# Performance work log

Hardware: AMD Instinct MI355X
Metric: run time of the kernel (lower is better)

## Reference

```python
import jax, jax.numpy as jnp
import numpy as np

TOP_K = 2
INIT_STD = 0.02
B, T, D, E, I = 2, 2048, 1024, 8, 512


def setup_inputs() -> dict:
    key = jax.random.key(0)
    k0, k1, k2, k3, k4 = jax.random.split(key, 5)
    return {
        "x": jax.random.normal(k0, (B, T, D), dtype=jnp.float32),
        "router_w": (jax.random.normal(k1, (E, D), dtype=jnp.float32) * INIT_STD),
        "w_gate": (jax.random.normal(k2, (E, I, D), dtype=jnp.float32) * INIT_STD),
        "w_up": (jax.random.normal(k3, (E, I, D), dtype=jnp.float32) * INIT_STD),
        "w_down": (jax.random.normal(k4, (E, D, I), dtype=jnp.float32) * INIT_STD),
    }


def _moe_forward(x, router_w, w_gate, w_up, w_down):
    # x: [B, T, D]; router_w: [E, D]; w_gate/w_up: [E, I, D]; w_down: [E, D, I]
    b, t, d = x.shape
    e = router_w.shape[0]
    gate_logits = jnp.einsum('btd,ed->bte', x, router_w)          # [B, T, E]
    top_w, sel = jax.lax.top_k(gate_logits, TOP_K)                # [B, T, K]
    probs = jax.nn.softmax(top_w, axis=-1)                        # softmax over selected experts only

    n = b * t
    xf = x.reshape(n, d)                                          # [N, D]
    sel_f = sel.reshape(n, TOP_K)
    probs_f = probs.reshape(n, TOP_K)
    # combine weights per (token, expert); zero for unselected experts
    gates = jnp.zeros((n, e), dtype=x.dtype).at[
        jnp.arange(n)[:, None], sel_f].add(probs_f)               # [N, E]

    # SwiGLU expert FFN (no bias). Gated-dense formulation: unselected experts
    # have gate weight exactly 0, so this is bit-for-bit the same math as
    # dispatch + grouped GEMM + combine. scan over experts keeps memory at
    # one [N, I] intermediate at a time.
    def body(acc, ws):
        wg, wu, wd, g = ws                                        # [I,D],[I,D],[D,I],[N]
        h = jax.nn.silu(xf @ wg.T) * (xf @ wu.T)                  # [N, I]
        return acc + g[:, None] * (h @ wd.T), None

    out, _ = jax.lax.scan(body, jnp.zeros((n, d), dtype=x.dtype),
                          (w_gate, w_up, w_down, gates.T))
    return out.reshape(b, t, d), gate_logits


def reference(x, router_w, w_gate, w_up, w_down):
    return _moe_forward(x, router_w, w_gate, w_up, w_down)
```

## Files before the change

### kernel.cpp

```cpp
#include <hip/hip_runtime.h>
#include <cstdint>

#define N_TOK 4096
#define D_    1024
#define E_    8
#define I_    512
#define KTOP  2
#define PAD   64
#define BK    64
#define CAP   (N_TOK*KTOP + E_*PAD)
#define NBX   (CAP / PAD)
#define WSZ   ((size_t)E_ * I_ * D_)

typedef __attribute__((ext_vector_type(4))) float f32x4;
typedef __attribute__((ext_vector_type(8))) short bf16x8;

__device__ inline unsigned short f2bf(float f) {
  union { float f; uint32_t u; } v; v.f = f;
  uint32_t r = v.u + 0x7fffu + ((v.u >> 16) & 1u);
  return (unsigned short)(r >> 16);
}
__device__ inline float bf2f(unsigned short h) {
  union { uint32_t u; float f; } v; v.u = ((uint32_t)h) << 16;
  return v.f;
}

#define GLOAD_LDS16(gp, lp)                                                        \
  __builtin_amdgcn_global_load_lds((const __attribute__((address_space(1))) void*)(gp), \
                                   (__attribute__((address_space(3))) void*)(lp), 16, 0, 0)

__global__ __launch_bounds__(256) void convertw_kernel(const float* __restrict__ wg,
                                                       const float* __restrict__ wu,
                                                       const float* __restrict__ wd,
                                                       unsigned short* __restrict__ dst) {
  const int y = blockIdx.y;
  const float* s = (y == 0) ? wg : (y == 1) ? wu : wd;
  unsigned short* d = dst + (size_t)y * WSZ;
  int i = blockIdx.x * 256 + threadIdx.x;
  const float4 v = reinterpret_cast<const float4*>(s)[i];
  ushort4 o;
  o.x = f2bf(v.x); o.y = f2bf(v.y); o.z = f2bf(v.z); o.w = f2bf(v.w);
  reinterpret_cast<ushort4*>(d)[i] = o;
}

__global__ __launch_bounds__(256) void router_kernel(const float* __restrict__ x,
                                                     const float* __restrict__ rw,
                                                     float* __restrict__ logits,
                                                     int* __restrict__ sel,
                                                     float* __restrict__ prob,
                                                     unsigned short* __restrict__ Xb) {
  const int lane = threadIdx.x & 63;
  const int tok  = blockIdx.x * 4 + (threadIdx.x >> 6);
  const float4* xr = reinterpret_cast<const float4*>(x + (size_t)tok * D_);
  float4 xv[4];
#pragma unroll
  for (int q = 0; q < 4; ++q) xv[q] = xr[q * 64 + lane];
  float acc[E_];
#pragma unroll
  for (int e = 0; e < E_; ++e) {
    const float4* wr = reinterpret_cast<const float4*>(rw + (size_t)e * D_);
    float s = 0.f;
#pragma unroll
    for (int q = 0; q < 4; ++q) {
      float4 wv = wr[q * 64 + lane];
      s += xv[q].x * wv.x + xv[q].y * wv.y + xv[q].z * wv.z + xv[q].w * wv.w;
    }
    acc[e] = s;
  }
  ushort4* xb = reinterpret_cast<ushort4*>(Xb + (size_t)tok * D_);
#pragma unroll
  for (int q = 0; q < 4; ++q) {
    ushort4 o;
    o.x = f2bf(xv[q].x); o.y = f2bf(xv[q].y); o.z = f2bf(xv[q].z); o.w = f2bf(xv[q].w);
    xb[q * 64 + lane] = o;
  }
#pragma unroll
  for (int e = 0; e < E_; ++e)
#pragma unroll
    for (int off = 32; off; off >>= 1) acc[e] += __shfl_xor(acc[e], off);
  if (lane == 0) {
    float v0 = -1e30f, v1 = -1e30f; int i0 = 0, i1 = 0;
#pragma unroll
    for (int e = 0; e < E_; ++e) {
      float v = acc[e];
      logits[(size_t)tok * E_ + e] = v;
      if (v > v0)      { v1 = v0; i1 = i0; v0 = v; i0 = e; }
      else if (v > v1) { v1 = v;  i1 = e; }
    }
    float t  = __expf(v1 - v0);
    sel[tok * 2] = i0; sel[tok * 2 + 1] = i1;
    prob[tok * 2] = 1.f / (1.f + t);
    prob[tok * 2 + 1] = t / (1.f + t);
  }
}

__global__ __launch_bounds__(1024) void plan_kernel(const int* __restrict__ sel,
                                                    const float* __restrict__ prob,
                                                    int* __restrict__ offs,
                                                    int* __restrict__ ptok,
                                                    float* __restrict__ pprob,
                                                    int* __restrict__ tpos,
                                                    unsigned int* __restrict__ zbuf) {
  __shared__ int wcnt[16][E_];
  __shared__ int pfx[16][E_];
  __shared__ int soffs[E_ + 1];
  __shared__ int secnt[E_];
  const int tid = threadIdx.x;
  const int wave = tid >> 6, lane = tid & 63;
  const unsigned long long lt = (1ull << lane) - 1ull;

  zbuf[tid] = 0u;

  int   mye[8];
  int   mylp[8];
  float myp[8];
  int run[E_];
#pragma unroll
  for (int e = 0; e < E_; ++e) run[e] = 0;

#pragma unroll
  for (int it = 0; it < 8; ++it) {
    int i = wave * 512 + it * 64 + lane;
    int e = sel[i];
    mye[it] = e;
    myp[it] = prob[i];
    int lp = 0;
#pragma unroll
    for (int ee = 0; ee < E_; ++ee) {
      unsigned long long m = __ballot(e == ee);
      if (e == ee) lp = run[ee] + __popcll(m & lt);
      run[ee] += __popcll(m);
    }
    mylp[it] = lp;
  }
#pragma unroll
  for (int ee = 0; ee < E_; ++ee)
    if (lane == ee) wcnt[wave][ee] = run[ee];
  __syncthreads();

  if (tid == 0) {
    int ro = 0;
#pragma unroll
    for (int e = 0; e < E_; ++e) {
      int c = 0;
      int r = ro;
      for (int w = 0; w < 16; ++w) { pfx[w][e] = r; r += wcnt[w][e]; c += wcnt[w][e]; }
      soffs[e] = ro; offs[e] = ro; secnt[e] = c;
      ro += (c + PAD - 1) & ~(PAD - 1);
    }
    soffs[E_] = ro; offs[E_] = ro;
  }
  __syncthreads();

#pragma unroll
  for (int it = 0; it < 8; ++it) {
    int i = wave * 512 + it * 64 + lane;
    int pos = pfx[wave][mye[it]] + mylp[it];
    ptok[pos]  = i >> 1;
    pprob[pos] = myp[it];
    tpos[i]    = pos;
  }
#pragma unroll
  for (int e = 0; e < E_; ++e) {
    int s = soffs[e] + secnt[e];
    int npad = soffs[e + 1] - s;
    if (tid < npad) { ptok[s + tid] = -1; pprob[s + tid] = 0.f; }
  }
}

__global__ __launch_bounds__(256, 4) void gemm1_kernel(const unsigned short* __restrict__ Xb,
                                                       const unsigned short* __restrict__ Wg,
                                                       const unsigned short* __restrict__ Wu,
                                                       const int* __restrict__ ptok,
                                                       const int* __restrict__ offs,
                                                       const unsigned short* __restrict__ zbuf,
                                                       unsigned short* __restrict__ H) {
  __shared__ unsigned short As[PAD * BK];
  __shared__ unsigned short Bg[64 * BK];
  __shared__ unsigned short Bu[64 * BK];
  __shared__ int toks[PAD];

  const int wgid = (blockIdx.x & 7) * 136 + (blockIdx.x >> 3);
  const int bx = wgid >> 3;
  const int by = wgid & 7;

  const int total = offs[E_];
  const int t0 = bx * PAD;
  if (t0 >= total) return;
  int e = 0;
#pragma unroll
  for (int i = 1; i < E_; ++i) if (offs[i] <= t0) e = i;

  const int tid  = threadIdx.x;
  const int lane = tid & 63;
  const int w    = tid >> 6;
  if (tid < PAD) toks[tid] = ptok[t0 + tid];
  __syncthreads();

  const int ib    = by * 64;
  const int gcol8 = (lane & 7) ^ (lane >> 3);

  const unsigned short* asrc[2];
  const unsigned short* bgsrc[2];
  const unsigned short* busrc[2];
#pragma unroll
  for (int i = 0; i < 2; ++i) {
    int r = w * 16 + i * 8 + (lane >> 3);
    int t = toks[r];
    asrc[i] = (t >= 0) ? (Xb + (size_t)t * D_ + gcol8 * 8) : (zbuf + gcol8 * 8);
    size_t rowoff = ((size_t)e * I_ + ib + r) * D_ + gcol8 * 8;
    bgsrc[i] = Wg + rowoff;
    busrc[i] = Wu + rowoff;
  }

  f32x4 accg[2][2], accu[2][2];
#pragma unroll
  for (int m = 0; m < 2; ++m)
#pragma unroll
    for (int n = 0; n < 2; ++n) {
      accg[m][n] = (f32x4){0.f, 0.f, 0.f, 0.f};
      accu[m][n] = (f32x4){0.f, 0.f, 0.f, 0.f};
    }

  const int wr = w >> 1, wc = w & 1;
  const int xr7 = lane & 7;

  for (int k0 = 0; k0 < D_; k0 += BK) {
#pragma unroll
    for (int i = 0; i < 2; ++i) {
      GLOAD_LDS16(asrc[i] + k0, &As[(w * 2 + i) * 512]);
      GLOAD_LDS16(bgsrc[i] + k0, &Bg[(w * 2 + i) * 512]);
      GLOAD_LDS16(busrc[i] + k0, &Bu[(w * 2 + i) * 512]);
    }
    __syncthreads();
#pragma unroll
    for (int kk = 0; kk < 2; ++kk) {
      const int uoff = ((kk * 4 + (lane >> 4)) ^ xr7) * 8;
      bf16x8 a[2], bg[2], bu[2];
#pragma unroll
      for (int m = 0; m < 2; ++m) {
        int row = wr * 32 + m * 16 + (lane & 15);
        a[m] = *reinterpret_cast<const bf16x8*>(&As[row * BK + uoff]);
      }
#pragma unroll
      for (int n = 0; n < 2; ++n) {
        int row = wc * 32 + n * 16 + (lane & 15);
        bg[n] = *reinterpret_cast<const bf16x8*>(&Bg[row * BK + uoff]);
        bu[n] = *reinterpret_cast<const bf16x8*>(&Bu[row * BK + uoff]);
      }
#pragma unroll
      for (int m = 0; m < 2; ++m)
#pragma unroll
        for (int n = 0; n < 2; ++n) {
          accg[m][n] = __builtin_amdgcn_mfma_f32_16x16x32_bf16(bg[n], a[m], accg[m][n], 0, 0, 0);
          accu[m][n] = __builtin_amdgcn_mfma_f32_16x16x32_bf16(bu[n], a[m], accu[m][n], 0, 0, 0);
        }
    }
    __syncthreads();
  }

#pragma unroll
  for (int m = 0; m < 2; ++m) {
    const int trow = wr * 32 + m * 16 + (lane & 15);
#pragma unroll
    for (int n = 0; n < 2; ++n) {
      const int icb = ib + wc * 32 + n * 16 + (lane >> 4) * 4;
      ushort4 st;
      float g, uu, h;
      g = accg[m][n][0]; uu = accu[m][n][0]; h = (g / (1.f + __expf(-g))) * uu; st.x = f2bf(h);
      g = accg[m][n][1]; uu = accu[m][n][1]; h = (g / (1.f + __expf(-g))) * uu; st.y = f2bf(h);
      g = accg[m][n][2]; uu = accu[m][n][2]; h = (g / (1.f + __expf(-g))) * uu; st.z = f2bf(h);
      g = accg[m][n][3]; uu = accu[m][n][3]; h = (g / (1.f + __expf(-g))) * uu; st.w = f2bf(h);
      *reinterpret_cast<ushort4*>(&H[(size_t)(t0 + trow) * I_ + icb]) = st;
    }
  }
}

__global__ __launch_bounds__(256, 4) void gemm2_kernel(const unsigned short* __restrict__ H,
                                                       const unsigned short* __restrict__ Wd,
                                                       const float* __restrict__ pprob,
                                                       const int* __restrict__ offs,
                                                       unsigned short* __restrict__ O) {
  __shared__ unsigned short As[PAD * BK];
  __shared__ unsigned short Bs[128 * BK];
  __shared__ float probs[PAD];

  const int wgid = (blockIdx.x & 7) * 136 + (blockIdx.x >> 3);
  const int bx = wgid >> 3;
  const int by = wgid & 7;

  const int total = offs[E_];
  const int t0 = bx * PAD;
  if (t0 >= total) return;
  int e = 0;
#pragma unroll
  for (int i = 1; i < E_; ++i) if (offs[i] <= t0) e = i;

  const int tid  = threadIdx.x;
  const int lane = tid & 63;
  const int w    = tid >> 6;
  if (tid < PAD) probs[tid] = pprob[t0 + tid];
  __syncthreads();

  const int db    = by * 128;
  const int gcol8 = (lane & 7) ^ (lane >> 3);

  const unsigned short* asrc[2];
#pragma unroll
  for (int i = 0; i < 2; ++i) {
    int r = w * 16 + i * 8 + (lane >> 3);
    asrc[i] = H + (size_t)(t0 + r) * I_ + gcol8 * 8;
  }
  const unsigned short* bsrc[4];
#pragma unroll
  for (int i = 0; i < 4; ++i) {
    int r = w * 32 + i * 8 + (lane >> 3);
    bsrc[i] = Wd + ((size_t)e * D_ + db + r) * I_ + gcol8 * 8;
  }

  f32x4 acc[2][4];
#pragma unroll
  for (int m = 0; m < 2; ++m)
#pragma unroll
    for (int n = 0; n < 4; ++n) acc[m][n] = (f32x4){0.f, 0.f, 0.f, 0.f};

  const int wr = w >> 1, wc = w & 1;
  const int xr7 = lane & 7;

  for (int k0 = 0; k0 < I_; k0 += BK) {
#pragma unroll
    for (int i = 0; i < 2; ++i) GLOAD_LDS16(asrc[i] + k0, &As[(w * 2 + i) * 512]);
#pragma unroll
    for (int i = 0; i < 4; ++i) GLOAD_LDS16(bsrc[i] + k0, &Bs[(w * 4 + i) * 512]);
    __syncthreads();
#pragma unroll
    for (int kk = 0; kk < 2; ++kk) {
      const int uoff = ((kk * 4 + (lane >> 4)) ^ xr7) * 8;
      bf16x8 a[2], b[4];
#pragma unroll
      for (int m = 0; m < 2; ++m) {
        int row = wr * 32 + m * 16 + (lane & 15);
        a[m] = *reinterpret_cast<const bf16x8*>(&As[row * BK + uoff]);
      }
#pragma unroll
      for (int n = 0; n < 4; ++n) {
        int row = wc * 64 + n * 16 + (lane & 15);
        b[n] = *reinterpret_cast<const bf16x8*>(&Bs[row * BK + uoff]);
      }
#pragma unroll
      for (int m = 0; m < 2; ++m)
#pragma unroll
        for (int n = 0; n < 4; ++n)
          acc[m][n] = __builtin_amdgcn_mfma_f32_16x16x32_bf16(b[n], a[m], acc[m][n], 0, 0, 0);
    }
    __syncthreads();
  }

#pragma unroll
  for (int m = 0; m < 2; ++m) {
    const int trow = wr * 32 + m * 16 + (lane & 15);
    const float p = probs[trow];
#pragma unroll
    for (int n = 0; n < 4; ++n) {
      const int dcb = db + wc * 64 + n * 16 + (lane >> 4) * 4;
      ushort4 v;
      v.x = f2bf(acc[m][n][0] * p); v.y = f2bf(acc[m][n][1] * p);
      v.z = f2bf(acc[m][n][2] * p); v.w = f2bf(acc[m][n][3] * p);
      *reinterpret_cast<ushort4*>(&O[(size_t)(t0 + trow) * D_ + dcb]) = v;
    }
  }
}

__global__ __launch_bounds__(256) void combine_kernel(const unsigned short* __restrict__ O,
                                                      const int* __restrict__ tpos,
                                                      float* __restrict__ out) {
  const int t = blockIdx.x;
  const int c = threadIdx.x;
  const int p0 = tpos[2 * t], p1 = tpos[2 * t + 1];
  const ushort4 a = reinterpret_cast<const ushort4*>(O + (size_t)p0 * D_)[c];
  const ushort4 b = reinterpret_cast<const ushort4*>(O + (size_t)p1 * D_)[c];
  float4 r;
  r.x = bf2f(a.x) + bf2f(b.x); r.y = bf2f(a.y) + bf2f(b.y);
  r.z = bf2f(a.z) + bf2f(b.z); r.w = bf2f(a.w) + bf2f(b.w);
  reinterpret_cast<float4*>(out + (size_t)t * D_)[c] = r;
}

extern "C" void kernel_launch(void* const* d_in, const int* in_sizes, int n_in,
                              void* d_out, int out_size, void* d_ws, size_t ws_size,
                              hipStream_t stream) {
  const float* x  = (const float*)d_in[0];
  const float* rw = (const float*)d_in[1];
  const float* wg = (const float*)d_in[2];
  const float* wu = (const float*)d_in[3];
  const float* wd = (const float*)d_in[4];
  float* out    = (float*)d_out;
  float* logits = out + (size_t)N_TOK * D_;

  char* ws = (char*)d_ws;
  int*   offs  = (int*)(ws + 64);
  unsigned short* zbuf = (unsigned short*)(ws + 256);
  int*   sel   = (int*)  (ws + 4352);
  float* prob  = (float*)(ws + 37120);
  int*   ptok  = (int*)  (ws + 69888);
  float* pprob = (float*)(ws + 104704);
  int*   tpos  = (int*)  (ws + 139520);
  unsigned short* Xb  = (unsigned short*)(ws + 172288);
  unsigned short* Wgb = Xb  + (size_t)N_TOK * D_;
  unsigned short* Wub = Wgb + WSZ;
  unsigned short* Wdb = Wub + WSZ;
  unsigned short* Hb  = Wdb + WSZ;
  unsigned short* Opos = Hb + (size_t)CAP * I_;

  convertw_kernel<<<dim3(WSZ / 4 / 256, 3), 256, 0, stream>>>(wg, wu, wd, Wgb);
  router_kernel<<<N_TOK / 4, 256, 0, stream>>>(x, rw, logits, sel, prob, Xb);
  plan_kernel<<<1, 1024, 0, stream>>>(sel, prob, offs, ptok, pprob, tpos, (unsigned int*)zbuf);
  gemm1_kernel<<<NBX * 8, 256, 0, stream>>>(Xb, Wgb, Wub, ptok, offs, zbuf, Hb);
  gemm2_kernel<<<NBX * 8, 256, 0, stream>>>(Hb, Wdb, pprob, offs, Opos);
  combine_kernel<<<N_TOK, 256, 0, stream>>>(Opos, tpos, out);
}
```

Measured before the change: 91.62 us.

## Fuse weight conversion into router kernel and convert w_down on the fly in gemm2

Folds the gate/up weight bf16 conversion and the router into one prep kernel, which drops a launch. The separate w_down conversion pass is removed. gemm2 now reads fp32 w_down directly, converts it in registers and writes the bf16 tile to LDS, using a double-buffered A tile and register prefetch of the next B tile. This avoids one write and one read of the full w_down copy, but gemm2 now reads fp32 weights (twice the bytes), repeated across token tiles, and converts them redundantly for every tile.

```diff
diff --git a/kernel.cpp b/kernel.cpp
--- a/kernel.cpp
+++ b/kernel.cpp
@@ -1,4 +1,5 @@
 #include <hip/hip_runtime.h>
+#include <hip/hip_bf16.h>
 #include <cstdint>
 
 #define N_TOK 4096
@@ -24,33 +25,39 @@
   union { uint32_t u; float f; } v; v.u = ((uint32_t)h) << 16;
   return v.f;
 }
+__device__ inline unsigned int pk2(float a, float b) {
+  __hip_bfloat162 h2 = __float22bfloat162_rn(float2{a, b});
+  return *reinterpret_cast<unsigned int*>(&h2);
+}
 
 #define GLOAD_LDS16(gp, lp)                                                        \
   __builtin_amdgcn_global_load_lds((const __attribute__((address_space(1))) void*)(gp), \
                                    (__attribute__((address_space(3))) void*)(lp), 16, 0, 0)
 
-__global__ __launch_bounds__(256) void convertw_kernel(const float* __restrict__ wg,
-                                                       const float* __restrict__ wu,
-                                                       const float* __restrict__ wd,
-                                                       unsigned short* __restrict__ dst) {
-  const int y = blockIdx.y;
-  const float* s = (y == 0) ? wg : (y == 1) ? wu : wd;
-  unsigned short* d = dst + (size_t)y * WSZ;
-  int i = blockIdx.x * 256 + threadIdx.x;
-  const float4 v = reinterpret_cast<const float4*>(s)[i];
-  ushort4 o;
-  o.x = f2bf(v.x); o.y = f2bf(v.y); o.z = f2bf(v.z); o.w = f2bf(v.w);
-  reinterpret_cast<ushort4*>(d)[i] = o;
-}
-
-__global__ __launch_bounds__(256) void router_kernel(const float* __restrict__ x,
-                                                     const float* __restrict__ rw,
-                                                     float* __restrict__ logits,
-                                                     int* __restrict__ sel,
-                                                     float* __restrict__ prob,
-                                                     unsigned short* __restrict__ Xb) {
+__global__ __launch_bounds__(256) void prep_kernel(const float* __restrict__ x,
+                                                   const float* __restrict__ rw,
+                                                   const float* __restrict__ wg,
+                                                   const float* __restrict__ wu,
+                                                   float* __restrict__ logits,
+                                                   int* __restrict__ sel,
+                                                   float* __restrict__ prob,
+                                                   unsigned short* __restrict__ Xb,
+                                                   unsigned short* __restrict__ Wb) {
+  int b = blockIdx.x;
+  if (b < 2 * 4096) {
+    const int y = b >> 12;
+    const float* s = (y == 0) ? wg : wu;
+    unsigned short* d = Wb + (size_t)y * WSZ;
+    const int i = (b & 4095) * 256 + threadIdx.x;
+    const float4 v = reinterpret_cast<const float4*>(s)[i];
+    ushort4 o;
+    o.x = f2bf(v.x); o.y = f2bf(v.y); o.z = f2bf(v.z); o.w = f2bf(v.w);
+    reinterpret_cast<ushort4*>(d)[i] = o;
+    return;
+  }
+  b -= 2 * 4096;
   const int lane = threadIdx.x & 63;
-  const int tok  = blockIdx.x * 4 + (threadIdx.x >> 6);
+  const int tok  = b * 4 + (threadIdx.x >> 6);
   const float4* xr = reinterpret_cast<const float4*>(x + (size_t)tok * D_);
   float4 xv[4];
 #pragma unroll
@@ -277,11 +284,11 @@
 }
 
 __global__ __launch_bounds__(256, 4) void gemm2_kernel(const unsigned short* __restrict__ H,
-                                                       const unsigned short* __restrict__ Wd,
+                                                       const float* __restrict__ Wd,
                                                        const float* __restrict__ pprob,
                                                        const int* __restrict__ offs,
                                                        unsigned short* __restrict__ O) {
-  __shared__ unsigned short As[PAD * BK];
+  __shared__ unsigned short As[2][PAD * BK];
   __shared__ unsigned short Bs[128 * BK];
   __shared__ float probs[PAD];
 
@@ -300,7 +307,6 @@
   const int lane = tid & 63;
   const int w    = tid >> 6;
   if (tid < PAD) probs[tid] = pprob[t0 + tid];
-  __syncthreads();
 
   const int db    = by * 128;
   const int gcol8 = (lane & 7) ^ (lane >> 3);
@@ -311,12 +317,12 @@
     int r = w * 16 + i * 8 + (lane >> 3);
     asrc[i] = H + (size_t)(t0 + r) * I_ + gcol8 * 8;
   }
-  const unsigned short* bsrc[4];
-#pragma unroll
-  for (int i = 0; i < 4; ++i) {
-    int r = w * 32 + i * 8 + (lane >> 3);
-    bsrc[i] = Wd + ((size_t)e * D_ + db + r) * I_ + gcol8 * 8;
-  }
+  const int brow = tid >> 1;
+  const float* bsrc = Wd + ((size_t)e * D_ + db + brow) * I_ + (tid & 1) * 32;
+  int bw[4];
+#pragma unroll
+  for (int j = 0; j < 4; ++j)
+    bw[j] = brow * 64 + ((((tid & 1) * 4 + j) ^ (brow & 7)) * 8);
 
   f32x4 acc[2][4];
 #pragma unroll
@@ -327,33 +333,65 @@
   const int wr = w >> 1, wc = w & 1;
   const int xr7 = lane & 7;
 
-  for (int k0 = 0; k0 < I_; k0 += BK) {
-#pragma unroll
-    for (int i = 0; i < 2; ++i) GLOAD_LDS16(asrc[i] + k0, &As[(w * 2 + i) * 512]);
-#pragma unroll
-    for (int i = 0; i < 4; ++i) GLOAD_LDS16(bsrc[i] + k0, &Bs[(w * 4 + i) * 512]);
-    __syncthreads();
-#pragma unroll
-    for (int kk = 0; kk < 2; ++kk) {
-      const int uoff = ((kk * 4 + (lane >> 4)) ^ xr7) * 8;
-      bf16x8 a[2], b[4];
-#pragma unroll
-      for (int m = 0; m < 2; ++m) {
-        int row = wr * 32 + m * 16 + (lane & 15);
-        a[m] = *reinterpret_cast<const bf16x8*>(&As[row * BK + uoff]);
-      }
-#pragma unroll
-      for (int n = 0; n < 4; ++n) {
-        int row = wc * 64 + n * 16 + (lane & 15);
-        b[n] = *reinterpret_cast<const bf16x8*>(&Bs[row * BK + uoff]);
-      }
-#pragma unroll
-      for (int m = 0; m < 2; ++m)
-#pragma unroll
-        for (int n = 0; n < 4; ++n)
-          acc[m][n] = __builtin_amdgcn_mfma_f32_16x16x32_bf16(b[n], a[m], acc[m][n], 0, 0, 0);
-    }
-    __syncthreads();
+  float4 bv[8];
+#define B_LOAD(k0)                                                             \
+  do {                                                                         \
+    _Pragma("unroll") for (int q = 0; q < 8; ++q)                              \
+        bv[q] = *reinterpret_cast<const float4*>(bsrc + (k0) + q * 4);         \
+  } while (0)
+#define B_CVT_WRITE                                                            \
+  do {                                                                         \
+    _Pragma("unroll") for (int j = 0; j < 4; ++j) {                            \
+      uint4 wv;                                                                \
+      wv.x = pk2(bv[2*j].x, bv[2*j].y);                                        \
+      wv.y = pk2(bv[2*j].z, bv[2*j].w);                                        \
+      wv.z = pk2(bv[2*j+1].x, bv[2*j+1].y);                                    \
+      wv.w = pk2(bv[2*j+1].z, bv[2*j+1].w);                                    \
+      *reinterpret_cast<uint4*>(&Bs[bw[j]]) = wv;                              \
+    }                                                                          \
+  } while (0)
+#define COMPUTE2(p)                                                            \
+  do {                                                                         \
+    _Pragma("unroll") for (int kk = 0; kk < 2; ++kk) {                         \
+      const int uoff = ((kk * 4 + (lane >> 4)) ^ xr7) * 8;                     \
+      bf16x8 a[2], bb[4];                                                      \
+      _Pragma("unroll") for (int m = 0; m < 2; ++m) {                          \
+        int row = wr * 32 + m * 16 + (lane & 15);                              \
+        a[m] = *reinterpret_cast<const bf16x8*>(&As[p][row * BK + uoff]);      \
+      }                                                                        \
+      _Pragma("unroll") for (int n = 0; n < 4; ++n) {                          \
+        int row = wc * 64 + n * 16 + (lane & 15);                              \
+        bb[n] = *reinterpret_cast<const bf16x8*>(&Bs[row * BK + uoff]);        \
+      }                                                                        \
+      _Pragma("unroll") for (int m = 0; m < 2; ++m)                            \
+        _Pragma("unroll") for (int n = 0; n < 4; ++n)                          \
+          acc[m][n] = __builtin_amdgcn_mfma_f32_16x16x32_bf16(bb[n], a[m], acc[m][n], 0, 0, 0); \
+    }                                                                          \
+  } while (0)
+
+  B_LOAD(0);
+#pragma unroll
+  for (int i = 0; i < 2; ++i) GLOAD_LDS16(asrc[i] + 0, &As[0][(w * 2 + i) * 512]);
+  B_CVT_WRITE;
+  __syncthreads();
+
+  const int NK = I_ / BK;
+  for (int t = 0; t < NK; ++t) {
+    const int p = t & 1;
+    if (t + 1 < NK) {
+      B_LOAD((t + 1) * BK);
+#pragma unroll
+      for (int i = 0; i < 2; ++i)
+        GLOAD_LDS16(asrc[i] + (t + 1) * BK, &As[p ^ 1][(w * 2 + i) * 512]);
+      __builtin_amdgcn_sched_barrier(0);
+    }
+    COMPUTE2(p);
+    if (t + 1 < NK) {
+      __builtin_amdgcn_sched_barrier(0);
+      __syncthreads();
+      B_CVT_WRITE;
+      __syncthreads();
+    }
   }
 
 #pragma unroll
@@ -369,6 +407,9 @@
       *reinterpret_cast<ushort4*>(&O[(size_t)(t0 + trow) * D_ + dcb]) = v;
     }
   }
+#undef B_LOAD
+#undef B_CVT_WRITE
+#undef COMPUTE2
 }
 
 __global__ __launch_bounds__(256) void combine_kernel(const unsigned short* __restrict__ O,
@@ -407,14 +448,13 @@
   unsigned short* Xb  = (unsigned short*)(ws + 172288);
   unsigned short* Wgb = Xb  + (size_t)N_TOK * D_;
   unsigned short* Wub = Wgb + WSZ;
-  unsigned short* Wdb = Wub + WSZ;
-  unsigned short* Hb  = Wdb + WSZ;
+  unsigned short* Hb  = Wub + WSZ;
   unsigned short* Opos = Hb + (size_t)CAP * I_;
 
-  convertw_kernel<<<dim3(WSZ / 4 / 256, 3), 256, 0, stream>>>(wg, wu, wd, Wgb);
-  router_kernel<<<N_TOK / 4, 256, 0, stream>>>(x, rw, logits, sel, prob, Xb);
+  prep_kernel<<<2 * 4096 + N_TOK / 4, 256, 0, stream>>>(x, rw, wg, wu,
+                                                        logits, sel, prob, Xb, Wgb);
   plan_kernel<<<1, 1024, 0, stream>>>(sel, prob, offs, ptok, pprob, tpos, (unsigned int*)zbuf);
   gemm1_kernel<<<NBX * 8, 256, 0, stream>>>(Xb, Wgb, Wub, ptok, offs, zbuf, Hb);
-  gemm2_kernel<<<NBX * 8, 256, 0, stream>>>(Hb, Wdb, pprob, offs, Opos);
+  gemm2_kernel<<<NBX * 8, 256, 0, stream>>>(Hb, wd, pprob, offs, Opos);
   combine_kernel<<<N_TOK, 256, 0, stream>>>(Opos, tpos, out);
 }
```

Result: slower. 119.4 us (+30.3%).
